# Kernel optimization log

Hardware: AMD Instinct MI355X
Metric: run time of the kernel (lower is better)

The kernel has to match this reference:

```python
import jax, jax.numpy as jnp
import numpy as np

STRIDES = (8, 16, 32)
FEATS = ((80, 80), (40, 40), (20, 20))  # 640x640 input, strides 8/16/32 -> 8400 points
NMS_THR = 0.65
SCORE_THR = 0.01


def _make_points():
    """MlvlPointGenerator.grid_priors with_stride=True, offset=0 (YOLOX)."""
    pts, strs = [], []
    for (h, w), s in zip(FEATS, STRIDES):
        ys, xs = jnp.meshgrid(jnp.arange(h, dtype=jnp.float32),
                              jnp.arange(w, dtype=jnp.float32), indexing='ij')
        pts.append(jnp.stack([xs.ravel() * s, ys.ravel() * s], axis=-1))
        strs.append(jnp.full((h * w,), float(s), jnp.float32))
    return jnp.concatenate(pts, axis=0), jnp.concatenate(strs, axis=0)


def _flatten(xs, c):
    # [N,C,H,W] per level -> [N, sum(H*W), C]
    return jnp.concatenate(
        [x.transpose(0, 2, 3, 1).reshape(x.shape[0], -1, c) for x in xs], axis=1)


def _pairwise_iou(b):
    # b: [N,4] x1y1x2y2 -> [N,N] IoU (torchvision box_iou convention, no +1)
    area = (b[:, 2] - b[:, 0]) * (b[:, 3] - b[:, 1])
    lt = jnp.maximum(b[:, None, :2], b[None, :, :2])
    rb = jnp.minimum(b[:, None, 2:], b[None, :, 2:])
    wh = jnp.clip(rb - lt, 0.0)
    inter = wh[..., 0] * wh[..., 1]
    return inter / jnp.maximum(area[:, None] + area[None, :] - inter, 1e-12)


def _nms_single(args):
    """bboxes_nms for one image; fixed-shape: returns score-sorted dets + keep mask."""
    cls, obj, boxes = args  # [N,C], [N], [N,4]
    max_scores = jnp.max(cls, axis=1)
    labels = jnp.argmax(cls, axis=1)
    scores = max_scores * obj
    valid = scores >= SCORE_THR
    # sort descending; invalid boxes get key -1 so they land at the end
    order = jnp.argsort(-jnp.where(valid, scores, -1.0))
    boxes_s = boxes[order]
    scores_s = scores[order]
    labels_s = labels[order]
    valid_s = valid[order]
    # batched_nms class-offset trick; NMS decisions are non-differentiable
    bng = jax.lax.stop_gradient(boxes_s)
    off = labels_s.astype(boxes.dtype) * (jnp.max(bng) + 1.0)
    iou = _pairwise_iou(bng + off[:, None])  # [N,N], dominant memory term
    n = boxes_s.shape[0]
    idx = jnp.arange(n)
    def body(i, keep):
        sup = keep[i] & (iou[i] > NMS_THR) & (idx > i)
        return keep & ~sup
    keep = jax.lax.fori_loop(0, n, body, valid_s)
    dets = jnp.concatenate([boxes_s, scores_s[:, None]], axis=-1)
    dets = dets * keep[:, None].astype(dets.dtype)  # zero out suppressed/invalid
    return dets, labels_s, keep


def reference(cls_out0, cls_out1, cls_out2, reg_out0, reg_out1, reg_out2,
              obj_out0, obj_out1, obj_out2):
    num_classes = cls_out0.shape[1]
    cls = jax.nn.sigmoid(_flatten([cls_out0, cls_out1, cls_out2], num_classes))  # [B,P,C]
    reg = _flatten([reg_out0, reg_out1, reg_out2], 4)                            # [B,P,4]
    obj = jax.nn.sigmoid(_flatten([obj_out0, obj_out1, obj_out2], 1))[..., 0]    # [B,P]
    points, strides = _make_points()                                             # [P,2],[P]
    # YOLOXBBoxDecoder
    xys = reg[..., :2] * strides[None, :, None] + points[None]
    whs = jnp.exp(reg[..., 2:]) * strides[None, :, None]
    boxes = jnp.concatenate([xys - whs * 0.5, xys + whs * 0.5], axis=-1)         # [B,P,4]
    # per-image NMS; lax.map keeps only one [P,P] IoU matrix live at a time
    return jax.lax.map(_nms_single, (cls, obj, boxes))


def setup_inputs() -> dict:
    key = jax.random.key(0)
    ks = jax.random.split(key, 9)
    B = 4
    shapes = {
        'cls_out0': (B, 80, 80, 80), 'cls_out1': (B, 80, 40, 40), 'cls_out2': (B, 80, 20, 20),
        'reg_out0': (B, 4, 80, 80),  'reg_out1': (B, 4, 40, 40),  'reg_out2': (B, 4, 20, 20),
        'obj_out0': (B, 1, 80, 80),  'obj_out1': (B, 1, 40, 40),  'obj_out2': (B, 1, 20, 20),
    }
    return {name: jax.random.normal(k, shp, dtype=jnp.float32)
            for k, (name, shp) in zip(ks, shapes.items())}
```

## Files before the change

kernel.cpp:

```cpp
#include <hip/hip_runtime.h>
#include <stdint.h>

#define NIMG 4
#define PTOT 8400
#define NCLS 80
#define NW   132
#define DMAX 3
#define NPAD 8448
#define ECAP 65536
#define ERCAP 1024
#define NMS_THR_C 0.65f
#define SCORE_THR_C 0.01f

static __device__ __forceinline__ float sigmoidf_(float x) {
  return 1.0f / (1.0f + expf(-x));
}
static __device__ __forceinline__ unsigned enc_f(float f) {
  unsigned u = __float_as_uint(f);
  return (u >> 31) ? ~u : (u | 0x80000000u);
}
static __device__ __forceinline__ float dec_f(unsigned e) {
  return (e >> 31) ? __uint_as_float(e ^ 0x80000000u) : __uint_as_float(~e);
}

__global__ void k_init(unsigned* gmax, uint64_t* flags, int* nvalid, int* lhist, int* ecnt) {
  int t = blockIdx.x * 256 + threadIdx.x;
  int NT = gridDim.x * 256;
  for (int k = t; k < NIMG * NW; k += NT) flags[k] = 0ull;
  for (int k = t; k < NIMG * NCLS; k += NT) lhist[k] = 0;
  if (t < NIMG) { gmax[t] = 0u; nvalid[t] = 0; ecnt[t] = 0; }
}

__global__ __launch_bounds__(256) void k_decode(
    const float* __restrict__ cls0, const float* __restrict__ cls1, const float* __restrict__ cls2,
    const float* __restrict__ reg0, const float* __restrict__ reg1, const float* __restrict__ reg2,
    const float* __restrict__ obj0, const float* __restrict__ obj1, const float* __restrict__ obj2,
    float* __restrict__ score, int* __restrict__ label, float* __restrict__ boxes,
    unsigned* __restrict__ gmax, int* __restrict__ lhist)
{
  int t = blockIdx.x * 256 + threadIdx.x;
  int n = t / (PTOT * 4);
  int rem = t - n * (PTOT * 4);
  int p = rem >> 2, q = rem & 3;
  const float* cb; const float* rb; const float* ob;
  int HW, W, pl; float s;
  if (p < 6400)      { cb = cls0; rb = reg0; ob = obj0; HW = 6400; W = 80; pl = p;        s = 8.f;  }
  else if (p < 8000) { cb = cls1; rb = reg1; ob = obj1; HW = 1600; W = 40; pl = p - 6400; s = 16.f; }
  else               { cb = cls2; rb = reg2; ob = obj2; HW = 400;  W = 20; pl = p - 8000; s = 32.f; }

  const float* cp = cb + (size_t)n * NCLS * HW + pl;
  float best = -1.0f; int bi = 0;
#pragma unroll
  for (int cc = 0; cc < 20; ++cc) {
    int c = q * 20 + cc;
    float v = sigmoidf_(cp[(size_t)c * HW]);
    if (v > best) { best = v; bi = c; }
  }
  {
    float ob_ = __shfl_xor(best, 1, 64); int oi = __shfl_xor(bi, 1, 64);
    float bl, bh; int il, ih;
    if ((q & 1) == 0) { bl = best; il = bi; bh = ob_; ih = oi; }
    else              { bl = ob_;  il = oi; bh = best; ih = bi; }
    if (bh > bl) { best = bh; bi = ih; } else { best = bl; bi = il; }
  }
  {
    float ob_ = __shfl_xor(best, 2, 64); int oi = __shfl_xor(bi, 2, 64);
    float bl, bh; int il, ih;
    if ((q & 2) == 0) { bl = best; il = bi; bh = ob_; ih = oi; }
    else              { bl = ob_;  il = oi; bh = best; ih = bi; }
    if (bh > bl) { best = bh; bi = ih; } else { best = bl; bi = il; }
  }

  float m = -3.4e38f;
  if (q == 0) {
    float osg = sigmoidf_(ob[(size_t)n * HW + pl]);
    float sc = best * osg;
    const float* rp = rb + (size_t)n * 4 * HW + pl;
    float rx = rp[0], ry = rp[(size_t)HW], rw = rp[(size_t)2 * HW], rh = rp[(size_t)3 * HW];
    int ph = pl / W, pw = pl - ph * W;
    float cx = rx * s + (float)pw * s, cy = ry * s + (float)ph * s;
    float bw = expf(rw) * s, bh2 = expf(rh) * s;
    float x1 = cx - bw * 0.5f, y1 = cy - bh2 * 0.5f;
    float x2 = cx + bw * 0.5f, y2 = cy + bh2 * 0.5f;
    int g = n * PTOT + p;
    score[g] = sc;
    label[g] = bi;
    atomicAdd(&lhist[n * NCLS + bi], 1);
    float* bx = boxes + (size_t)g * 4;
    bx[0] = x1; bx[1] = y1; bx[2] = x2; bx[3] = y2;
    m = fmaxf(fmaxf(x1, y1), fmaxf(x2, y2));
  }
  for (int o = 32; o; o >>= 1) m = fmaxf(m, __shfl_xor(m, o, 64));
  if ((threadIdx.x & 63) == 0) atomicMax(&gmax[n], enc_f(m));
}

__global__ __launch_bounds__(256) void k_sort(
    const float* __restrict__ score, int* __restrict__ rank,
    const int* __restrict__ lhist, int* __restrict__ bstart, int* __restrict__ cursor)
{
  __shared__ uint32_t A[NPAD];
  __shared__ uint16_t Pp[NPAD];
  __shared__ uint16_t hist[16 * 256];
  __shared__ uint32_t part[256];
  __shared__ uint32_t wsum[4];
  int n = blockIdx.x, t = threadIdx.x;
  const float* sc = score + (size_t)n * PTOT;
  for (int i = t; i < PTOT; i += 256) {
    float v = sc[i];
    float key = (v >= SCORE_THR_C) ? v : -1.0f;
    A[i] = ~enc_f(key);
    Pp[i] = (uint16_t)i;
  }
  for (int i = PTOT + t; i < NPAD; i += 256) {
    A[i] = 0xFFFFFFFFu;
    Pp[i] = (uint16_t)i;
  }
  __syncthreads();
  const int base0 = t * 33;
  for (int pass = 0; pass < 8; ++pass) {
    const int sh = pass * 4;
    uint32_t k[33]; uint16_t p[33];
#pragma unroll
    for (int e = 0; e < 33; ++e) { k[e] = A[base0 + e]; p[e] = Pp[base0 + e]; }
    uint64_t c0 = 0, c1 = 0;
#pragma unroll
    for (int e = 0; e < 33; ++e) {
      uint32_t d = (k[e] >> sh) & 15u;
      uint64_t inc = 1ull << ((d & 7u) << 3);
      if (d < 8) c0 += inc; else c1 += inc;
    }
#pragma unroll
    for (int d = 0; d < 16; ++d) {
      uint32_t cnt = (uint32_t)(((d < 8) ? (c0 >> (d * 8)) : (c1 >> ((d - 8) * 8))) & 0xFFull);
      hist[d * 256 + t] = (uint16_t)cnt;
    }
    __syncthreads();
    uint32_t s = 0;
#pragma unroll
    for (int qq = 0; qq < 16; ++qq) {
      int f = t * 16 + qq;
      uint32_t h = hist[f];
      hist[f] = (uint16_t)s;
      s += h;
    }
    uint32_t v = s;
#pragma unroll
    for (int off = 1; off < 64; off <<= 1) {
      uint32_t u = __shfl_up(v, off, 64);
      if ((t & 63) >= off) v += u;
    }
    if ((t & 63) == 63) wsum[t >> 6] = v;
    __syncthreads();
    uint32_t wpre = 0;
#pragma unroll
    for (int wv = 0; wv < 4; ++wv) wpre += (wv < (t >> 6)) ? wsum[wv] : 0;
    part[t] = v - s + wpre;
    __syncthreads();
    uint64_t cc0 = 0, cc1 = 0;
#pragma unroll
    for (int e = 0; e < 33; ++e) {
      uint32_t d = (k[e] >> sh) & 15u;
      int f = d * 256 + t;
      uint32_t within = (uint32_t)(((d < 8) ? (cc0 >> ((d & 7u) << 3))
                                            : (cc1 >> ((d & 7u) << 3))) & 0xFFull);
      uint32_t pos = (uint32_t)hist[f] + part[f >> 4] + within;
      A[pos] = k[e];
      Pp[pos] = p[e];
      uint64_t inc = 1ull << ((d & 7u) << 3);
      if (d < 8) cc0 += inc; else cc1 += inc;
    }
    __syncthreads();
  }
  for (int pos = t; pos < PTOT; pos += 256)
    rank[(size_t)n * PTOT + Pp[pos]] = pos;
  if (t == 0) {
    int acc = 0;
    for (int L = 0; L < NCLS; ++L) { bstart[n * (NCLS + 1) + L] = acc; acc += lhist[n * NCLS + L]; }
    bstart[n * (NCLS + 1) + NCLS] = acc;
  }
  __syncthreads();
  if (t < NCLS) cursor[n * NCLS + t] = bstart[n * (NCLS + 1) + t];
}

__global__ __launch_bounds__(256) void k_scatter(
    const float* __restrict__ score, const int* __restrict__ label, const float* __restrict__ boxes,
    const unsigned* __restrict__ gmax, const int* __restrict__ rank, int* __restrict__ nvalid,
    float* __restrict__ s_score, int* __restrict__ s_label,
    float* __restrict__ s_box, float* __restrict__ s_sbox, float* __restrict__ s_area,
    int* __restrict__ cursor, int* __restrict__ bidx)
{
  int n = blockIdx.y;
  int i = blockIdx.x * 256 + threadIdx.x;
  if (i >= PTOT) return;
  const float* sc = score + (size_t)n * PTOT;
  float v = sc[i];
  bool valid = (v >= SCORE_THR_C);
  unsigned long long bal = __ballot(valid);
  if ((threadIdx.x & 63) == 0) atomicAdd(&nvalid[n], (int)__popcll(bal));

  int r = rank[(size_t)n * PTOT + i];
  float gm = dec_f(gmax[n]);
  int li = label[(size_t)n * PTOT + i];
  const float* bp = boxes + ((size_t)n * PTOT + i) * 4;
  float b0 = bp[0], b1 = bp[1], b2 = bp[2], b3 = bp[3];
  float off = (float)li * (gm + 1.0f);
  float q0 = b0 + off, q1 = b1 + off, q2 = b2 + off, q3 = b3 + off;
  float area = (q2 - q0) * (q3 - q1);

  size_t d = (size_t)n * PTOT + (size_t)r;
  s_score[d] = v;
  s_label[d] = li;
  float* sb = s_box + d * 4;  sb[0] = b0; sb[1] = b1; sb[2] = b2; sb[3] = b3;
  float* sq = s_sbox + d * 4; sq[0] = q0; sq[1] = q1; sq[2] = q2; sq[3] = q3;
  s_area[d] = area;
  int pos = atomicAdd(&cursor[n * NCLS + li], 1);
  bidx[(size_t)n * PTOT + pos] = r;
}

__global__ __launch_bounds__(256) void k_pairs(
    const float* __restrict__ s_sbox, const float* __restrict__ s_area,
    const int* __restrict__ bstart, const int* __restrict__ bidx,
    uint32_t* __restrict__ eb, int* __restrict__ ecnt, uint64_t* __restrict__ flags)
{
  int n = blockIdx.z, L = blockIdx.x, d = blockIdx.y;
  int L2 = L + d;
  if (L2 >= NCLS) return;
  const int* bs = bstart + n * (NCLS + 1);
  int a0 = bs[L], a1 = bs[L + 1];
  int b0 = bs[L2], b1 = bs[L2 + 1];
  int na = a1 - a0, nb = b1 - b0;
  if (na == 0 || nb == 0) return;
  const int* ba = bidx + (size_t)n * PTOT + a0;
  const int* bb = bidx + (size_t)n * PTOT + b0;
  const float4* SB = (const float4*)(s_sbox + (size_t)n * PTOT * 4);
  const float* SA = s_area + (size_t)n * PTOT;
  int tot = na * nb;
  for (int t = threadIdx.x; t < tot; t += 256) {
    int u = t / nb, v = t - u * nb;
    if (d == 0 && u >= v) continue;
    int p = ba[u], q = bb[v];
    float4 A = SB[p], B = SB[q];
    float ww = fminf(A.z, B.z) - fmaxf(A.x, B.x);
    float hh = fminf(A.w, B.w) - fmaxf(A.y, B.y);
    if (ww <= 0.0f || hh <= 0.0f) continue;
    float inter = ww * hh;
    float aa = SA[p], ab = SA[q];
    float uni = fmaxf(aa + ab - inter, 1e-12f);
    if (inter / uni > NMS_THR_C) {
      uint32_t i = (uint32_t)min(p, q), j = (uint32_t)max(p, q);
      int idx = atomicAdd(&ecnt[n], 1);
      if (idx < ECAP) eb[(size_t)n * ECAP + idx] = (i << 16) | j;
      atomicOr((unsigned long long*)&flags[(size_t)n * NW + (i >> 6)], 1ull << (i & 63u));
    }
  }
}

__global__ __launch_bounds__(64) void k_scan(
    const uint32_t* __restrict__ eb, const int* __restrict__ ecnt,
    const uint64_t* __restrict__ flags, const int* __restrict__ nvalid,
    uint64_t* __restrict__ keepw)
{
  __shared__ uint64_t Rm[NW];
  __shared__ uint64_t Fl[NW];
  int n = blockIdx.x, l = threadIdx.x;
  int nv = nvalid[n];
  auto initw = [&](int w) -> uint64_t {
    int base = w * 64;
    if (nv <= base) return ~0ull;
    if (nv >= base + 64) return 0ull;
    return (~0ull) << (nv - base);
  };
  const uint64_t* fl = flags + (size_t)n * NW;
  uint64_t f0 = fl[l], f1 = fl[64 + l], f2 = (l < 4) ? fl[128 + l] : 0ull;
  Rm[l] = initw(l); Rm[64 + l] = initw(64 + l);
  if (l < 4) Rm[128 + l] = initw(128 + l);
  Fl[l] = f0; Fl[64 + l] = f1;
  if (l < 4) Fl[128 + l] = f2;
  uint64_t nzc0 = __ballot(f0 != 0ull);
  uint64_t nzc1 = __ballot(f1 != 0ull);
  uint64_t nzc2 = __ballot((l < 4) && (f2 != 0ull));
  int cnt = ecnt[n]; if (cnt > ECAP) cnt = ECAP;
  const uint32_t* E = eb + (size_t)n * ECAP;
  uint32_t Er[16];
#pragma unroll
  for (int s = 0; s < 16; ++s) {
    int k = s * 64 + l;
    Er[s] = (k < cnt) ? E[k] : 0xFFFFFFFFu;
  }
  for (int seg = 0; seg < 3; ++seg) {
    uint64_t bm = (seg == 0) ? nzc0 : (seg == 1) ? nzc1 : nzc2;
    int cb = seg * 64;
    while (bm) {
      int c = cb + __builtin_ctzll(bm); bm &= bm - 1;
      uint64_t F = Fl[c];
      while (F) {
        int b = __builtin_ctzll(F); F &= F - 1;
        uint64_t cur = Rm[c];
        if ((cur >> b) & 1ull) continue;
        uint32_t i = (uint32_t)(c * 64 + b);
#pragma unroll
        for (int s = 0; s < 16; ++s) {
          uint32_t e = Er[s];
          if ((e >> 16) == i) {
            uint32_t j = e & 0xFFFFu;
            atomicOr((unsigned long long*)&Rm[j >> 6], 1ull << (j & 63u));
          }
        }
        if (cnt > ERCAP) {
          for (int k = ERCAP + l; k < cnt; k += 64) {
            uint32_t e = E[k];
            if ((e >> 16) == i) {
              uint32_t j = e & 0xFFFFu;
              atomicOr((unsigned long long*)&Rm[j >> 6], 1ull << (j & 63u));
            }
          }
        }
      }
    }
  }
  keepw[(size_t)n * NW + l] = ~Rm[l];
  keepw[(size_t)n * NW + 64 + l] = ~Rm[64 + l];
  if (l < 4) keepw[(size_t)n * NW + 128 + l] = ~Rm[128 + l];
}

__global__ __launch_bounds__(256) void k_final(
    const float* __restrict__ s_score, const int* __restrict__ s_label,
    const float* __restrict__ s_box, const uint64_t* __restrict__ keepw,
    float* __restrict__ out)
{
  int t = blockIdx.x * 256 + threadIdx.x;
  if (t >= NIMG * PTOT) return;
  int n = t / PTOT, p = t - n * PTOT;
  uint64_t w = keepw[(size_t)n * NW + (p >> 6)];
  float k = (float)((w >> (p & 63)) & 1ull);
  float* dets = out;
  float* lab  = out + (size_t)NIMG * PTOT * 5;
  float* kp   = out + (size_t)NIMG * PTOT * 6;
  const float* bp = s_box + (size_t)t * 4;
  float* dp = dets + (size_t)t * 5;
  dp[0] = bp[0] * k; dp[1] = bp[1] * k; dp[2] = bp[2] * k; dp[3] = bp[3] * k;
  dp[4] = s_score[t] * k;
  lab[t] = (float)s_label[t];
  kp[t]  = k;
}

extern "C" void kernel_launch(void* const* d_in, const int* in_sizes, int n_in,
                              void* d_out, int out_size, void* d_ws, size_t ws_size,
                              hipStream_t stream)
{
  const float* cls0 = (const float*)d_in[0];
  const float* cls1 = (const float*)d_in[1];
  const float* cls2 = (const float*)d_in[2];
  const float* reg0 = (const float*)d_in[3];
  const float* reg1 = (const float*)d_in[4];
  const float* reg2 = (const float*)d_in[5];
  const float* obj0 = (const float*)d_in[6];
  const float* obj1 = (const float*)d_in[7];
  const float* obj2 = (const float*)d_in[8];

  char* w = (char*)d_ws;
  uint64_t* keepw = (uint64_t*)w; w += (size_t)NIMG * NW * 8;
  uint64_t* flags = (uint64_t*)w; w += (size_t)NIMG * NW * 8;
  float* score = (float*)w;       w += (size_t)NIMG * PTOT * 4;
  int*   label = (int*)w;         w += (size_t)NIMG * PTOT * 4;
  float* boxes = (float*)w;       w += (size_t)NIMG * PTOT * 16;
  float* ss = (float*)w;          w += (size_t)NIMG * PTOT * 4;
  int*   sl = (int*)w;            w += (size_t)NIMG * PTOT * 4;
  float* sb = (float*)w;          w += (size_t)NIMG * PTOT * 16;
  float* sq = (float*)w;          w += (size_t)NIMG * PTOT * 16;
  float* sa = (float*)w;          w += (size_t)NIMG * PTOT * 4;
  unsigned* gmax = (unsigned*)w;  w += 256;
  int* nvalid = (int*)w;          w += 256;
  int* rank = (int*)w;            w += (size_t)NIMG * PTOT * 4;
  int* lhist = (int*)w;           w += (size_t)NIMG * NCLS * 4;
  int* bstart = (int*)w;          w += (size_t)NIMG * (NCLS + 1) * 4;
  int* cursor = (int*)w;          w += (size_t)NIMG * NCLS * 4;
  int* bidx = (int*)w;            w += (size_t)NIMG * PTOT * 4;
  uint32_t* eb = (uint32_t*)w;    w += (size_t)NIMG * ECAP * 4;
  int* ecnt = (int*)w;            w += 256;

  k_init<<<dim3(4), dim3(256), 0, stream>>>(gmax, flags, nvalid, lhist, ecnt);
  k_decode<<<dim3((NIMG * PTOT * 4) / 256), dim3(256), 0, stream>>>(
      cls0, cls1, cls2, reg0, reg1, reg2, obj0, obj1, obj2,
      score, label, boxes, gmax, lhist);
  k_sort<<<dim3(NIMG), dim3(256), 0, stream>>>(score, rank, lhist, bstart, cursor);
  k_scatter<<<dim3((PTOT + 255) / 256, NIMG), dim3(256), 0, stream>>>(
      score, label, boxes, gmax, rank, nvalid, ss, sl, sb, sq, sa, cursor, bidx);
  k_pairs<<<dim3(NCLS, DMAX + 1, NIMG), dim3(256), 0, stream>>>(
      sq, sa, bstart, bidx, eb, ecnt, flags);
  k_scan<<<dim3(NIMG), dim3(64), 0, stream>>>(eb, ecnt, flags, nvalid, keepw);
  k_final<<<dim3((NIMG * PTOT + 255) / 256), dim3(256), 0, stream>>>(
      ss, sl, sb, keepw, (float*)d_out);
}
```

Measured before the change: 209.2 us.

## Tile class-pair IoU into shared memory and skip unreachable class offsets

k_pairs now stages each class bucket's boxes, areas and indices into LDS tiles of 512 and loops the outer box serially with the inner boxes across threads. This replaces the per-pair gathered global loads and the integer division used to split the flattened pair index. k_decode also tracks a per-image minimum coordinate, which lets k_pairs skip cross-class blocks whose class offset cannot be overlapped given the box coordinate range. The tradeoff is extra barriers and a serial outer loop, which may underuse threads when buckets are small.

```diff
diff --git a/kernel.cpp b/kernel.cpp
--- a/kernel.cpp
+++ b/kernel.cpp
@@ -9,6 +9,7 @@
 #define NPAD 8448
 #define ECAP 65536
 #define ERCAP 1024
+#define PTILE 512
 #define NMS_THR_C 0.65f
 #define SCORE_THR_C 0.01f
 
@@ -23,12 +24,13 @@
   return (e >> 31) ? __uint_as_float(e ^ 0x80000000u) : __uint_as_float(~e);
 }
 
-__global__ void k_init(unsigned* gmax, uint64_t* flags, int* nvalid, int* lhist, int* ecnt) {
+__global__ void k_init(unsigned* gmax, unsigned* gmin, uint64_t* flags, int* nvalid,
+                       int* lhist, int* ecnt) {
   int t = blockIdx.x * 256 + threadIdx.x;
   int NT = gridDim.x * 256;
   for (int k = t; k < NIMG * NW; k += NT) flags[k] = 0ull;
   for (int k = t; k < NIMG * NCLS; k += NT) lhist[k] = 0;
-  if (t < NIMG) { gmax[t] = 0u; nvalid[t] = 0; ecnt[t] = 0; }
+  if (t < NIMG) { gmax[t] = 0u; gmin[t] = 0xFFFFFFFFu; nvalid[t] = 0; ecnt[t] = 0; }
 }
 
 __global__ __launch_bounds__(256) void k_decode(
@@ -36,7 +38,7 @@
     const float* __restrict__ reg0, const float* __restrict__ reg1, const float* __restrict__ reg2,
     const float* __restrict__ obj0, const float* __restrict__ obj1, const float* __restrict__ obj2,
     float* __restrict__ score, int* __restrict__ label, float* __restrict__ boxes,
-    unsigned* __restrict__ gmax, int* __restrict__ lhist)
+    unsigned* __restrict__ gmax, unsigned* __restrict__ gmin, int* __restrict__ lhist)
 {
   int t = blockIdx.x * 256 + threadIdx.x;
   int n = t / (PTOT * 4);
@@ -71,7 +73,7 @@
     if (bh > bl) { best = bh; bi = ih; } else { best = bl; bi = il; }
   }
 
-  float m = -3.4e38f;
+  float m = -3.4e38f, m2 = 3.4e38f;
   if (q == 0) {
     float osg = sigmoidf_(ob[(size_t)n * HW + pl]);
     float sc = best * osg;
@@ -88,10 +90,17 @@
     atomicAdd(&lhist[n * NCLS + bi], 1);
     float* bx = boxes + (size_t)g * 4;
     bx[0] = x1; bx[1] = y1; bx[2] = x2; bx[3] = y2;
-    m = fmaxf(fmaxf(x1, y1), fmaxf(x2, y2));
-  }
-  for (int o = 32; o; o >>= 1) m = fmaxf(m, __shfl_xor(m, o, 64));
-  if ((threadIdx.x & 63) == 0) atomicMax(&gmax[n], enc_f(m));
+    m = fmaxf(x2, y2);
+    m2 = fminf(x1, y1);
+  }
+  for (int o = 32; o; o >>= 1) {
+    m = fmaxf(m, __shfl_xor(m, o, 64));
+    m2 = fminf(m2, __shfl_xor(m2, o, 64));
+  }
+  if ((threadIdx.x & 63) == 0) {
+    atomicMax(&gmax[n], enc_f(m));
+    atomicMin(&gmin[n], enc_f(m2));
+  }
 }
 
 __global__ __launch_bounds__(256) void k_sort(
@@ -220,37 +229,63 @@
 __global__ __launch_bounds__(256) void k_pairs(
     const float* __restrict__ s_sbox, const float* __restrict__ s_area,
     const int* __restrict__ bstart, const int* __restrict__ bidx,
+    const unsigned* __restrict__ gmax, const unsigned* __restrict__ gmin,
     uint32_t* __restrict__ eb, int* __restrict__ ecnt, uint64_t* __restrict__ flags)
 {
   int n = blockIdx.z, L = blockIdx.x, d = blockIdx.y;
   int L2 = L + d;
   if (L2 >= NCLS) return;
+  if (d > 0) {
+    float gm = dec_f(gmax[n]), gmn = dec_f(gmin[n]);
+    if ((float)d * (gm + 1.0f) > (gm - gmn) + 1.0f) return;
+  }
   const int* bs = bstart + n * (NCLS + 1);
-  int a0 = bs[L], a1 = bs[L + 1];
-  int b0 = bs[L2], b1 = bs[L2 + 1];
-  int na = a1 - a0, nb = b1 - b0;
+  int a0 = bs[L], na = bs[L + 1] - a0;
+  int b0 = bs[L2], nb = bs[L2 + 1] - b0;
   if (na == 0 || nb == 0) return;
   const int* ba = bidx + (size_t)n * PTOT + a0;
   const int* bb = bidx + (size_t)n * PTOT + b0;
   const float4* SB = (const float4*)(s_sbox + (size_t)n * PTOT * 4);
   const float* SA = s_area + (size_t)n * PTOT;
-  int tot = na * nb;
-  for (int t = threadIdx.x; t < tot; t += 256) {
-    int u = t / nb, v = t - u * nb;
-    if (d == 0 && u >= v) continue;
-    int p = ba[u], q = bb[v];
-    float4 A = SB[p], B = SB[q];
-    float ww = fminf(A.z, B.z) - fmaxf(A.x, B.x);
-    float hh = fminf(A.w, B.w) - fmaxf(A.y, B.y);
-    if (ww <= 0.0f || hh <= 0.0f) continue;
-    float inter = ww * hh;
-    float aa = SA[p], ab = SA[q];
-    float uni = fmaxf(aa + ab - inter, 1e-12f);
-    if (inter / uni > NMS_THR_C) {
-      uint32_t i = (uint32_t)min(p, q), j = (uint32_t)max(p, q);
-      int idx = atomicAdd(&ecnt[n], 1);
-      if (idx < ECAP) eb[(size_t)n * ECAP + idx] = (i << 16) | j;
-      atomicOr((unsigned long long*)&flags[(size_t)n * NW + (i >> 6)], 1ull << (i & 63u));
+
+  __shared__ float4 lA[PTILE]; __shared__ float lAa[PTILE]; __shared__ int liA[PTILE];
+  __shared__ float4 lB[PTILE]; __shared__ float lBa[PTILE]; __shared__ int liB[PTILE];
+  int tid = threadIdx.x;
+
+  for (int ub = 0; ub < na; ub += PTILE) {
+    int ua = min(PTILE, na - ub);
+    for (int i = tid; i < ua; i += 256) {
+      int p = ba[ub + i];
+      liA[i] = p; lA[i] = SB[p]; lAa[i] = SA[p];
+    }
+    for (int vb = 0; vb < nb; vb += PTILE) {
+      int va = min(PTILE, nb - vb);
+      for (int i = tid; i < va; i += 256) {
+        int p = bb[vb + i];
+        liB[i] = p; lB[i] = SB[p]; lBa[i] = SA[p];
+      }
+      __syncthreads();
+      for (int u = 0; u < ua; ++u) {
+        float4 A = lA[u]; float aa = lAa[u]; int p = liA[u];
+        int vstart = 0;
+        if (d == 0) { vstart = (ub + u) + 1 - vb; if (vstart < 0) vstart = 0; }
+        for (int v = vstart + tid; v < va; v += 256) {
+          float4 B = lB[v];
+          float ww = fminf(A.z, B.z) - fmaxf(A.x, B.x);
+          float hh = fminf(A.w, B.w) - fmaxf(A.y, B.y);
+          if (ww <= 0.0f || hh <= 0.0f) continue;
+          float inter = ww * hh;
+          float uni = fmaxf(aa + lBa[v] - inter, 1e-12f);
+          if (inter / uni > NMS_THR_C) {
+            uint32_t q = (uint32_t)liB[v];
+            uint32_t i_ = min((uint32_t)p, q), j_ = max((uint32_t)p, q);
+            int idx = atomicAdd(&ecnt[n], 1);
+            if (idx < ECAP) eb[(size_t)n * ECAP + idx] = (i_ << 16) | j_;
+            atomicOr((unsigned long long*)&flags[(size_t)n * NW + (i_ >> 6)], 1ull << (i_ & 63u));
+          }
+        }
+      }
+      __syncthreads();
     }
   }
 }
@@ -370,6 +405,7 @@
   float* sq = (float*)w;          w += (size_t)NIMG * PTOT * 16;
   float* sa = (float*)w;          w += (size_t)NIMG * PTOT * 4;
   unsigned* gmax = (unsigned*)w;  w += 256;
+  unsigned* gmin = (unsigned*)w;  w += 256;
   int* nvalid = (int*)w;          w += 256;
   int* rank = (int*)w;            w += (size_t)NIMG * PTOT * 4;
   int* lhist = (int*)w;           w += (size_t)NIMG * NCLS * 4;
@@ -379,15 +415,15 @@
   uint32_t* eb = (uint32_t*)w;    w += (size_t)NIMG * ECAP * 4;
   int* ecnt = (int*)w;            w += 256;
 
-  k_init<<<dim3(4), dim3(256), 0, stream>>>(gmax, flags, nvalid, lhist, ecnt);
+  k_init<<<dim3(4), dim3(256), 0, stream>>>(gmax, gmin, flags, nvalid, lhist, ecnt);
   k_decode<<<dim3((NIMG * PTOT * 4) / 256), dim3(256), 0, stream>>>(
       cls0, cls1, cls2, reg0, reg1, reg2, obj0, obj1, obj2,
-      score, label, boxes, gmax, lhist);
+      score, label, boxes, gmax, gmin, lhist);
   k_sort<<<dim3(NIMG), dim3(256), 0, stream>>>(score, rank, lhist, bstart, cursor);
   k_scatter<<<dim3((PTOT + 255) / 256, NIMG), dim3(256), 0, stream>>>(
       score, label, boxes, gmax, rank, nvalid, ss, sl, sb, sq, sa, cursor, bidx);
   k_pairs<<<dim3(NCLS, DMAX + 1, NIMG), dim3(256), 0, stream>>>(
-      sq, sa, bstart, bidx, eb, ecnt, flags);
+      sq, sa, bstart, bidx, gmax, gmin, eb, ecnt, flags);
   k_scan<<<dim3(NIMG), dim3(64), 0, stream>>>(eb, ecnt, flags, nvalid, keepw);
   k_final<<<dim3((NIMG * PTOT + 255) / 256), dim3(256), 0, stream>>>(
       ss, sl, sb, keepw, (float*)d_out);
```

After: 196.7 us. 1.06x faster.
